# Performance work log

Hardware: AMD Instinct MI355X
Metric: run time of the kernel (lower is better)

## Reference

```python
import jax, jax.numpy as jnp
import numpy as np

B, T = 256, 1024
IN_DIM, OUT_DIM = 32, 32
STATE_DIM, DIM_NL = 128, 128
EPS = 1e-3            # pos_def_tol
ALPHA = 1.0           # contraction_rate_lb
STD = 0.5             # initialization_std


def setup_inputs() -> dict:
    key = jax.random.key(0)
    ks = jax.random.split(key, 9)
    f = lambda k, sh: jax.random.normal(k, sh, dtype=jnp.float32)
    n, q = STATE_DIM, DIM_NL
    return {
        "x0_sys": f(ks[0], (B, 1, OUT_DIM)),
        "u_in": f(ks[1], (B, T, IN_DIM)),
        "X": f(ks[2], (2 * n + q, 2 * n + q)) * STD,
        "Y": f(ks[3], (n, n)) * STD,
        "B2": f(ks[4], (n, IN_DIM)) * STD,
        "C2": f(ks[5], (OUT_DIM, n)) * STD,
        "D21": f(ks[6], (OUT_DIM, q)) * STD,
        "D22": f(ks[7], (OUT_DIM, IN_DIM)) * STD,
        "D12": f(ks[8], (q, IN_DIM)) * STD,
    }


def _derived(X, Y):
    # Contraction-preserving reparametrization ("_update_model_param").
    n, q = STATE_DIM, DIM_NL
    H = X.T @ X + EPS * jnp.eye(2 * n + q, dtype=X.dtype)
    H11 = H[:n, :n]
    H21 = H[n:n + q, :n]
    H22 = H[n:n + q, n:n + q]
    H31 = H[n + q:, :n]
    H32 = H[n + q:, n:n + q]
    H33 = H[n + q:, n + q:]          # P
    F_ = H31
    B1 = H32
    E = 0.5 * (H11 + ALPHA * H33 + Y - Y.T)
    E_inv = jnp.linalg.inv(E)
    Lam = 0.5 * jnp.diag(H22)
    D11 = -jnp.tril(H22, -1)          # strictly lower triangular
    C1 = -H21
    return F_, B1, E_inv, Lam, D11, C1


def reference(x0_sys, u_in, X, Y, B2, C2, D21, D22, D12):
    F_, B1, E_inv, Lam, D11, C1 = _derived(X, Y)
    q = DIM_NL

    # reset(): x0 = min-norm lstsq solution of C2 x0 = y0_sys  (lstsq == pinv here)
    y0_sys = x0_sys[:, 0, :]                       # (B, out)
    x0 = (jnp.linalg.pinv(C2) @ y0_sys.T).T        # (B, n)
    y0 = x0 @ C2.T                                 # (B, out)

    idx = jnp.arange(q)

    def step(x, u):
        # one REN forward step; x:(B,n), u:(B,in)
        a = x @ C1.T + u @ D12.T                   # (B, q), i-independent part of v

        def inner(w, inp):
            i, d_row, lam, a_i = inp               # a_i:(B,)
            v = a_i + w @ d_row                    # strictly-lower-tri recurrence on w
            return w.at[:, i].set(jnp.tanh(v / lam)), None

        w0 = jnp.zeros((x.shape[0], q), x.dtype)
        w, _ = jax.lax.scan(inner, w0, (idx, D11, Lam, a.T))
        x_new = (x @ F_.T + w @ B1.T + u @ B2.T) @ E_inv.T
        y = x_new @ C2.T + w @ D21.T + u @ D22.T
        return x_new, y

    _, ys = jax.lax.scan(step, x0, jnp.swapaxes(u_in, 0, 1))   # (T, B, out)
    # run() emits y0 then outputs after u[0..T-2] (last step's y is dropped)
    y_traj = jnp.concatenate([y0[None], ys[:-1]], axis=0)      # (T, B, out)
    return jnp.swapaxes(y_traj, 0, 1)                          # (B, T, out)
```

## Files before the change

### kernel.cpp

```cpp
#include <hip/hip_runtime.h>
#include <hip/hip_bf16.h>

#define DEV static __device__ __forceinline__

constexpr int Tn = 1024;
constexpr float LOG2E = 1.4426950408889634f;

constexpr int OFF_H     = 0;
constexpr int OFF_E     = 147456;
constexpr int OFF_EINV  = 163840;
constexpr int OFF_M     = 180224;
constexpr int OFF_MINV  = 181248;
constexpr int OFF_GL2   = 182272;
constexpr int OFF_FH    = 182400;
constexpr int OFF_B1H   = 198784;
constexpr int OFF_B2H   = 215168;
constexpr int OFF_W0    = 219264;
constexpr int OFF_WC    = 223360;
constexpr int OFF_CF    = 227456;
constexpr int OFF_CB    = 243840;
constexpr int OFF_CB2   = 260224;
constexpr int OFF_PF    = 264320;
constexpr int OFF_PB    = 280704;
constexpr int OFF_PCF   = 297088;
constexpr int OFF_PCB   = 313472;
constexpr int OFF_SAB   = 329856;
constexpr int OFF_SB2   = 338048;
constexpr int OFF_BUQ   = 342144;
constexpr int OFF_D12Q  = 346240;
constexpr int OFF_SCB2  = 350336;
constexpr int OFF_WCS   = 354432;
constexpr int OFF_C2Y   = 358528;
constexpr int OFF_D21Y  = 362624;
constexpr int OFF_D22Y  = 366720;
constexpr int OFF_AUG   = 367744;
constexpr int OFF_AUG2  = 400512;
constexpr int OFF_X0    = 402560;
constexpr int OFF_A0    = 435328;
constexpr int WS_FLOATS = 468096;

__device__ __align__(16) float g_ws[WS_FLOATS];
__device__ int g_isf32;

DEV float ld(const void* p, size_t i, int f) {
  return f ? ((const float*)p)[i]
           : __bfloat162float(((const __hip_bfloat16*)p)[i]);
}
DEV float rdlane(float v, int l) {
  return __int_as_float(__builtin_amdgcn_readlane(__float_as_int(v), l));
}

__global__ void k_detect(const void* __restrict__ X) {
  if (threadIdx.x == 0) {
    const __hip_bfloat16* p = (const __hip_bfloat16*)X;
    int bad = 0;
    for (int i = 0; i < 512; ++i) {
      float v = __bfloat162float(p[i]);
      if (!(v > -1e6f && v < 1e6f)) bad++;
    }
    g_isf32 = (bad > 0) ? 1 : 0;
  }
}

__global__ void k_H(const void* __restrict__ X) {
  const int f = g_isf32;
  float* ws = g_ws;
  int id = blockIdx.x * 256 + threadIdx.x;
  int r = id / 384, c = id % 384;
  float acc = 0.f;
  for (int k = 0; k < 384; ++k)
    acc = fmaf(ld(X, k * 384 + r, f), ld(X, k * 384 + c, f), acc);
  if (r == c) acc += 0.001f;
  ws[OFF_H + id] = acc;
}

__global__ void k_derived(const void* __restrict__ Y, const void* __restrict__ C2) {
  const int f = g_isf32;
  float* ws = g_ws;
  const float* H = ws + OFF_H;
  int id = blockIdx.x * 256 + threadIdx.x;
  if (id < 16384) {
    int i = id >> 7, j = id & 127;
    ws[OFF_E + id] = 0.5f * (H[i * 384 + j] + H[(256 + i) * 384 + 256 + j]
                             + ld(Y, i * 128 + j, f) - ld(Y, j * 128 + i, f));
  } else if (id < 16512) {
    int i = id - 16384;
    ws[OFF_GL2 + i] = LOG2E * 4.f / H[(128 + i) * 384 + 128 + i];
  } else if (id < 17536) {
    int t = id - 16512; int a = t >> 5, b = t & 31;
    float acc = 0.f;
    for (int j = 0; j < 128; ++j)
      acc = fmaf(ld(C2, a * 128 + j, f), ld(C2, b * 128 + j, f), acc);
    ws[OFF_M + t] = acc;
  }
}

__global__ void k_inv_lds() {
  extern __shared__ float smv[];
  float* aug  = smv;
  float* aug2 = smv + 32768;
  __shared__ float col[128];
  float* ws = g_ws;
  const float* E = ws + OFF_E;
  int tid = threadIdx.x;
  for (int idx = tid; idx < 32768; idx += 1024) {
    int i = idx >> 8, j = idx & 255;
    aug[idx] = (j < 128) ? E[i * 128 + j] : ((j - 128) == i ? 1.f : 0.f);
  }
  __syncthreads();
  for (int k = 0; k < 128; ++k) {
    if (tid < 128) col[tid] = aug[tid * 256 + k];
    __syncthreads();
    float d = 1.f / col[k];
    if (tid < 256) aug[k * 256 + tid] *= d;
    __syncthreads();
    int j = tid & 255, iseg = tid >> 8;
    float rkj = aug[k * 256 + j];
    for (int i = iseg * 32; i < iseg * 32 + 32; ++i) {
      if (i == k) continue;
      aug[i * 256 + j] -= col[i] * rkj;
    }
    __syncthreads();
  }
  for (int idx = tid; idx < 16384; idx += 1024) {
    int i = idx >> 7, j = idx & 127;
    ws[OFF_EINV + idx] = aug[i * 256 + 128 + j];
  }
  const float* M = ws + OFF_M;
  for (int idx = tid; idx < 2048; idx += 1024) {
    int i = idx >> 6, j = idx & 63;
    aug2[idx] = (j < 32) ? M[i * 32 + j] : ((j - 32) == i ? 1.f : 0.f);
  }
  __syncthreads();
  for (int k = 0; k < 32; ++k) {
    if (tid < 32) col[tid] = aug2[tid * 64 + k];
    __syncthreads();
    float d = 1.f / col[k];
    if (tid < 64) aug2[k * 64 + tid] *= d;
    __syncthreads();
    if (tid < 64) {
      float rkj = aug2[k * 64 + tid];
      for (int i = 0; i < 32; ++i) if (i != k) aug2[i * 64 + tid] -= col[i] * rkj;
    }
    __syncthreads();
  }
  for (int idx = tid; idx < 1024; idx += 1024) {
    int i = idx >> 5, j = idx & 31;
    ws[OFF_MINV + idx] = aug2[i * 64 + 32 + j];
  }
}

__global__ void k_inv() {
  float* ws = g_ws;
  __shared__ float col[128];
  float* aug = ws + OFF_AUG;
  const float* E = ws + OFF_E;
  int tid = threadIdx.x;
  for (int idx = tid; idx < 32768; idx += 1024) {
    int i = idx >> 8, j = idx & 255;
    aug[idx] = (j < 128) ? E[i * 128 + j] : ((j - 128) == i ? 1.f : 0.f);
  }
  __syncthreads();
  for (int k = 0; k < 128; ++k) {
    if (tid < 128) col[tid] = aug[tid * 256 + k];
    __syncthreads();
    float d = 1.f / col[k];
    if (tid < 256) aug[k * 256 + tid] *= d;
    __syncthreads();
    int j = tid & 255, iseg = tid >> 8;
    float rkj = aug[k * 256 + j];
    for (int i = iseg * 32; i < iseg * 32 + 32; ++i) {
      if (i == k) continue;
      aug[i * 256 + j] -= col[i] * rkj;
    }
    __syncthreads();
  }
  for (int idx = tid; idx < 16384; idx += 1024) {
    int i = idx >> 7, j = idx & 127;
    ws[OFF_EINV + idx] = aug[i * 256 + 128 + j];
  }
  __syncthreads();
  float* aug2 = ws + OFF_AUG2;
  const float* M = ws + OFF_M;
  for (int idx = tid; idx < 2048; idx += 1024) {
    int i = idx >> 6, j = idx & 63;
    aug2[idx] = (j < 32) ? M[i * 32 + j] : ((j - 32) == i ? 1.f : 0.f);
  }
  __syncthreads();
  for (int k = 0; k < 32; ++k) {
    if (tid < 32) col[tid] = aug2[tid * 64 + k];
    __syncthreads();
    float d = 1.f / col[k];
    if (tid < 64) aug2[k * 64 + tid] *= d;
    __syncthreads();
    if (tid < 64) {
      float rkj = aug2[k * 64 + tid];
      for (int i = 0; i < 32; ++i) if (i != k) aug2[i * 64 + tid] -= col[i] * rkj;
    }
    __syncthreads();
  }
  for (int idx = tid; idx < 1024; idx += 1024) {
    int i = idx >> 5, j = idx & 31;
    ws[OFF_MINV + idx] = aug2[i * 64 + 32 + j];
  }
}

__global__ void k_fuse(const void* __restrict__ B2, const void* __restrict__ C2) {
  const int f = g_isf32;
  float* ws = g_ws;
  const float* einv = ws + OFF_EINV;
  const float* H = ws + OFF_H;
  const float* minv = ws + OFF_MINV;
  int id = blockIdx.x * 256 + threadIdx.x;
  if (id < 16384) {
    int l = id >> 7, j = id & 127;
    float a = 0.f;
    for (int m = 0; m < 128; ++m) a = fmaf(einv[l * 128 + m], H[(256 + m) * 384 + j], a);
    ws[OFF_FH + id] = a;
  } else if (id < 32768) {
    int t = id - 16384; int l = t >> 7, j = t & 127;
    float a = 0.f;
    for (int m = 0; m < 128; ++m) a = fmaf(einv[l * 128 + m], H[(256 + m) * 384 + 128 + j], a);
    ws[OFF_B1H + t] = a;
  } else if (id < 36864) {
    int t = id - 32768; int l = t >> 5, k = t & 31;
    float a = 0.f;
    for (int m = 0; m < 128; ++m) a = fmaf(einv[l * 128 + m], ld(B2, m * 32 + k, f), a);
    ws[OFF_B2H + t] = a;
  } else if (id < 40960) {
    int t = id - 36864; int k = t >> 7, l = t & 127;
    float a = 0.f;
    for (int m = 0; m < 32; ++m) a = fmaf(minv[k * 32 + m], ld(C2, m * 128 + l, f), a);
    ws[OFF_W0 + t] = a;
  }
}

__global__ void k_w2() {
  float* ws = g_ws;
  const float* H = ws + OFF_H;
  const float* w0 = ws + OFF_W0;
  int id = blockIdx.x * 256 + threadIdx.x;
  int k = id >> 7, l = id & 127;
  float a = 0.f;
  for (int m = 0; m < 128; ++m) a = fmaf(w0[k * 128 + m], -H[(128 + l) * 384 + m], a);
  ws[OFF_WC + id] = a;
}

__global__ void k_cf() {
  float* ws = g_ws;
  const float* H = ws + OFF_H;
  int id = blockIdx.x * 256 + threadIdx.x;
  if (id < 16384) {
    int l = id >> 7, j = id & 127;
    float a = 0.f;
    for (int m = 0; m < 128; ++m) a = fmaf(-H[(128 + l) * 384 + m], ws[OFF_FH + m * 128 + j], a);
    ws[OFF_CF + id] = a;
  } else if (id < 32768) {
    int t = id - 16384; int l = t >> 7, j = t & 127;
    float a = 0.f;
    for (int m = 0; m < 128; ++m) a = fmaf(-H[(128 + l) * 384 + m], ws[OFF_B1H + m * 128 + j], a);
    ws[OFF_CB + t] = a;
  } else {
    int t = id - 32768; int l = t >> 5, k = t & 31;
    float a = 0.f;
    for (int m = 0; m < 128; ++m) a = fmaf(-H[(128 + l) * 384 + m], ws[OFF_B2H + m * 32 + k], a);
    ws[OFF_CB2 + t] = a;
  }
}

__global__ void k_pk(const void* __restrict__ D12, const void* __restrict__ C2,
                     const void* __restrict__ D21, const void* __restrict__ D22) {
  const int f = g_isf32;
  float* ws = g_ws;
  const float* H = ws + OFF_H;
  const float* g = ws + OFF_GL2;
  int id = blockIdx.x * 256 + threadIdx.x;
  if (id < 8192) {
    int j = id >> 6, l = id & 63;
    ((float2*)(ws + OFF_PF))[id] =
        make_float2(ws[OFF_FH + l * 128 + j], ws[OFF_FH + (l + 64) * 128 + j]);
  } else if (id < 16384) {
    int t = id - 8192; int j = t >> 6, l = t & 63;
    ((float2*)(ws + OFF_PB))[t] =
        make_float2(ws[OFF_B1H + l * 128 + j], ws[OFF_B1H + (l + 64) * 128 + j]);
  } else if (id < 24576) {
    int t = id - 16384; int j = t >> 6, l = t & 63;
    ((float2*)(ws + OFF_PCF))[t] =
        make_float2(g[l] * ws[OFF_CF + l * 128 + j], g[l + 64] * ws[OFF_CF + (l + 64) * 128 + j]);
  } else if (id < 32768) {
    int t = id - 24576; int j = t >> 6, l = t & 63;
    ((float2*)(ws + OFF_PCB))[t] =
        make_float2(g[l] * ws[OFF_CB + l * 128 + j], g[l + 64] * ws[OFF_CB + (l + 64) * 128 + j]);
  } else if (id < 36864) {
    int t = id - 32768; int i = t >> 6, l = t & 63;
    float sx = (i < l) ? -g[l] * H[(128 + l) * 384 + 128 + i] : 0.f;
    float sy = -g[l + 64] * H[(192 + l) * 384 + 128 + i];
    ((float2*)(ws + OFF_SAB))[t] = make_float2(sx, sy);
  } else if (id < 40960) {
    int t = id - 36864; int ii = t >> 6, l = t & 63;
    ws[OFF_SB2 + t] = (ii < l) ? -g[l + 64] * H[(192 + l) * 384 + 192 + ii] : 0.f;
  } else if (id < 43008) {
    int t = id - 40960; int k = t >> 6, l = t & 63;
    ((float2*)(ws + OFF_BUQ))[t] =
        make_float2(ws[OFF_B2H + l * 32 + k], ws[OFF_B2H + (l + 64) * 32 + k]);
  } else if (id < 45056) {
    int t = id - 43008; int k = t >> 6, l = t & 63;
    ((float2*)(ws + OFF_D12Q))[t] =
        make_float2(g[l] * ld(D12, l * 32 + k, f), g[l + 64] * ld(D12, (l + 64) * 32 + k, f));
  } else if (id < 47104) {
    int t = id - 45056; int k = t >> 6, l = t & 63;
    ((float2*)(ws + OFF_SCB2))[t] =
        make_float2(g[l] * ws[OFF_CB2 + l * 32 + k], g[l + 64] * ws[OFF_CB2 + (l + 64) * 32 + k]);
  } else if (id < 49152) {
    int t = id - 47104; int k = t >> 6, l = t & 63;
    ((float2*)(ws + OFF_WCS))[t] =
        make_float2(g[l] * ws[OFF_WC + k * 128 + l], g[l + 64] * ws[OFF_WC + k * 128 + l + 64]);
  } else if (id < 53248) {
    int t = id - 49152; int m = t >> 5, o = t & 31;
    ws[OFF_C2Y + t] = ld(C2, o * 128 + m, f);
  } else if (id < 57344) {
    int t = id - 53248; int m = t >> 5, o = t & 31;
    ws[OFF_D21Y + t] = ld(D21, o * 128 + m, f);
  } else if (id < 58368) {
    int t = id - 57344; int k = t >> 5, o = t & 31;
    ws[OFF_D22Y + t] = ld(D22, o * 32 + k, f);
  }
}

__global__ void k_x0a0(const void* __restrict__ x0s, const void* __restrict__ u_in) {
  const int f = g_isf32;
  float* ws = g_ws;
  int id = blockIdx.x * 256 + threadIdx.x;
  if (id < 32768) {
    int b = id >> 7, l = id & 127;
    float a = 0.f;
    for (int k = 0; k < 32; ++k)
      a = fmaf(ld(x0s, b * 32 + k, f), ws[OFF_W0 + k * 128 + l], a);
    ws[OFF_X0 + id] = a;
  } else {
    int t = id - 32768; int b = t >> 6, lane = t & 63;
    const float2* WCs = (const float2*)(ws + OFF_WCS);
    const float2* D12Q = (const float2*)(ws + OFF_D12Q);
    float ax = 0.f, ay = 0.f;
    for (int k = 0; k < 32; ++k) {
      float yk = ld(x0s, b * 32 + k, f);
      float2 wc = WCs[k * 64 + lane];
      ax = fmaf(wc.x, yk, ax); ay = fmaf(wc.y, yk, ay);
      float u0 = ld(u_in, b * Tn * 32 + k, f);
      float2 dq = D12Q[k * 64 + lane];
      ax = fmaf(dq.x, u0, ax); ay = fmaf(dq.y, u0, ay);
    }
    ((float2*)(ws + OFF_A0))[b * 64 + lane] = make_float2(ax, ay);
  }
}

DEV void y_emit(const float* ws, float xlv, float xhv, float2 wv, float uyv,
                int b, int t, int lane, int f, void* out) {
  int o = lane & 31, h = lane >> 5;
  const float* C2Y = ws + OFF_C2Y;
  const float* D21Y = ws + OFF_D21Y;
  const float* D22Y = ws + OFF_D22Y;
  float acc = 0.f;
#pragma unroll 8
  for (int l = 0; l < 64; ++l) {
    float xle = rdlane(xlv, l), xhe = rdlane(xhv, l);
    float xv = h ? xhe : xle;
    acc = fmaf(xv, C2Y[(l + 64 * h) * 32 + o], acc);
  }
#pragma unroll 8
  for (int l = 0; l < 64; ++l) {
    float wxe = rdlane(wv.x, l), wye = rdlane(wv.y, l);
    float wvv = h ? wye : wxe;
    acc = fmaf(wvv, D21Y[(l + 64 * h) * 32 + o], acc);
  }
  if (h == 0) {
#pragma unroll 8
    for (int k = 0; k < 32; ++k)
      acc = fmaf(rdlane(uyv, k), D22Y[k * 32 + o], acc);
  }
  acc += __shfl_down(acc, 32);
  if (lane < 32) {
    size_t oi = ((size_t)b * Tn + t) * 32 + o;
    if (f) ((float*)out)[oi] = acc;
    else   ((__hip_bfloat16*)out)[oi] = __float2bfloat16(acc);
  }
}

__global__ __launch_bounds__(512) void k_scan8(const void* __restrict__ u_in,
                                               const void* __restrict__ x0s,
                                               void* __restrict__ out) {
  __shared__ float2 sSAB[64 * 64];
  __shared__ float  sSB2[64 * 64];
  __shared__ float2 xbuf[2][8][64];
  __shared__ float2 abuf[2][8][64];
  const float* ws = g_ws;
  const int f = g_isf32;
  const int tid = threadIdx.x, lane = tid & 63, w = tid >> 6;
  for (int i = tid; i < 4096; i += 512) sSAB[i] = ((const float2*)(ws + OFF_SAB))[i];
  for (int i = tid; i < 4096; i += 512) sSB2[i] = ws[OFF_SB2 + i];

  const int b = blockIdx.x;
  const bool isScan = (w < 4);

  float2 vA[32], vB[32];
  if (isScan) {
    const float2* P1 = (const float2*)(ws + OFF_PB);
    const float2* P2 = (const float2*)(ws + OFF_PCB);
    const int jcol = (w & 3) * 32;
#pragma unroll
    for (int c = 0; c < 32; ++c) {
      vA[c] = P1[(jcol + c) * 64 + lane];
      vB[c] = P2[(jcol + c) * 64 + lane];
    }
  }
  float xl = ws[OFF_X0 + b * 128 + lane];
  float xh = ws[OFF_X0 + b * 128 + 64 + lane];
  float2 a2 = ((const float2*)(ws + OFF_A0))[b * 64 + lane];
  float accx = a2.x, accy = a2.y;

  float ucur = 0.f;
  float u0v = 0.f, u1v = 0.f;
  float uyc = 0.f;
  if (w == 4 && lane < 32) ucur = ld(u_in, (size_t)b * Tn * 32 + lane, f);
  if (w == 6 && lane < 32) {
    u0v = ld(u_in, (size_t)b * Tn * 32 + lane, f);
    u1v = ld(u_in, ((size_t)b * Tn + 1) * 32 + lane, f);
  }
  if (w == 6) { xbuf[0][6][lane] = make_float2(0.f, 0.f); xbuf[1][6][lane] = make_float2(0.f, 0.f); }
  if (w == 7 && lane < 32) {
    size_t oi = (size_t)b * Tn * 32 + lane;
    float v = ld(x0s, b * 32 + lane, f);
    if (f) ((float*)out)[oi] = v;
    else   ((__hip_bfloat16*)out)[oi] = __float2bfloat16(v);
  }
  const int jb = __builtin_amdgcn_readfirstlane((w & 1) * 32);
  __syncthreads();

#pragma unroll 1
  for (int t = 0; t < Tn - 1; ++t) {
    const int p = t & 1;
    if (isScan) {
      __builtin_amdgcn_s_setprio(1);
#pragma unroll
      for (int i = 0; i < 64; ++i) {
        float s = rdlane(accx, i);
        float e2 = __builtin_amdgcn_exp2f(s);
        float wi = fmaf(-2.f, __builtin_amdgcn_rcpf(1.f + e2), 1.f);
        float2 sp = sSAB[i * 64 + lane];
        accx = fmaf(sp.x, wi, accx);
        accy = fmaf(sp.y, wi, accy);
      }
      float ex = __builtin_amdgcn_exp2f(accx);
      float wx = fmaf(-2.f, __builtin_amdgcn_rcpf(1.f + ex), 1.f);
#pragma unroll
      for (int i = 0; i < 64; ++i) {
        float s = rdlane(accy, i);
        float e2 = __builtin_amdgcn_exp2f(s);
        float wi = fmaf(-2.f, __builtin_amdgcn_rcpf(1.f + e2), 1.f);
        accy = fmaf(sSB2[i * 64 + lane], wi, accy);
      }
      float ey = __builtin_amdgcn_exp2f(accy);
      float wy = fmaf(-2.f, __builtin_amdgcn_rcpf(1.f + ey), 1.f);
      if (w == 0) xbuf[p][7][lane] = make_float2(wx, wy);

      float px = 0.f, py = 0.f, pax = 0.f, pay = 0.f;
      float wsrc = (w < 2) ? wx : wy;
#pragma unroll
      for (int c = 0; c < 32; ++c) {
        float wj = rdlane(wsrc, jb + c);
        px  = fmaf(vA[c].x, wj, px);
        py  = fmaf(vA[c].y, wj, py);
        pax = fmaf(vB[c].x, wj, pax);
        pay = fmaf(vB[c].y, wj, pay);
      }
      __builtin_amdgcn_s_setprio(0);
      if (w != 0) xbuf[p][w][lane] = make_float2(px, py);
      else        xbuf[p][0][lane] = make_float2(px, py);
      abuf[p][w][lane] = make_float2(pax, pay);
      __syncthreads();
      float sax = 0.f, say = 0.f;
#pragma unroll
      for (int w2 = 0; w2 < 7; ++w2) {
        float2 av = abuf[p][w2][lane];
        sax += av.x; say += av.y;
      }
      accx = sax; accy = say;
    } else if (w == 4) {
      float un = ucur;
      if (lane < 32) un = ld(u_in, ((size_t)b * Tn + t + 1) * 32 + lane, f);
      float px = 0.f, py = 0.f, pax = 0.f, pay = 0.f;
      const float2* BUq = (const float2*)(ws + OFF_BUQ);
#pragma unroll 8
      for (int k = 0; k < 32; ++k) {
        float uk = rdlane(ucur, k);
        float2 bu = BUq[k * 64 + lane];
        px = fmaf(bu.x, uk, px); py = fmaf(bu.y, uk, py);
      }
      const float2* PF = (const float2*)(ws + OFF_PF);
      const float2* PCF = (const float2*)(ws + OFF_PCF);
#pragma unroll 8
      for (int c = 0; c < 64; ++c) {
        float xj = rdlane(xl, c);
        float2 fv = PF[c * 64 + lane];
        float2 cv = PCF[c * 64 + lane];
        px  = fmaf(fv.x, xj, px);  py  = fmaf(fv.y, xj, py);
        pax = fmaf(cv.x, xj, pax); pay = fmaf(cv.y, xj, pay);
      }
      ucur = un;
      xbuf[p][4][lane] = make_float2(px, py);
      abuf[p][4][lane] = make_float2(pax, pay);
      __syncthreads();
      float sxl = 0.f, sxh = 0.f;
#pragma unroll
      for (int w2 = 0; w2 < 7; ++w2) {
        float2 xv = xbuf[p][w2][lane];
        sxl += xv.x; sxh += xv.y;
      }
      xl = sxl; xh = sxh;
    } else if (w == 5) {
      float px = 0.f, py = 0.f, pax = 0.f, pay = 0.f;
      const float2* PF = (const float2*)(ws + OFF_PF);
      const float2* PCF = (const float2*)(ws + OFF_PCF);
#pragma unroll 8
      for (int c = 0; c < 64; ++c) {
        float xj = rdlane(xh, c);
        float2 fv = PF[(64 + c) * 64 + lane];
        float2 cv = PCF[(64 + c) * 64 + lane];
        px  = fmaf(fv.x, xj, px);  py  = fmaf(fv.y, xj, py);
        pax = fmaf(cv.x, xj, pax); pay = fmaf(cv.y, xj, pay);
      }
      xbuf[p][5][lane] = make_float2(px, py);
      abuf[p][5][lane] = make_float2(pax, pay);
      __syncthreads();
      float sxl = 0.f, sxh = 0.f;
#pragma unroll
      for (int w2 = 0; w2 < 7; ++w2) {
        float2 xv = xbuf[p][w2][lane];
        sxl += xv.x; sxh += xv.y;
      }
      xl = sxl; xh = sxh;
    } else if (w == 6) {
      float u2v = u1v;
      if (lane < 32 && t + 2 < Tn) u2v = ld(u_in, ((size_t)b * Tn + t + 2) * 32 + lane, f);
      float pax = 0.f, pay = 0.f;
      const float2* SC = (const float2*)(ws + OFF_SCB2);
      const float2* DQ = (const float2*)(ws + OFF_D12Q);
#pragma unroll 8
      for (int k = 0; k < 32; ++k) {
        float u0k = rdlane(u0v, k);
        float2 sc = SC[k * 64 + lane];
        pax = fmaf(sc.x, u0k, pax); pay = fmaf(sc.y, u0k, pay);
        float u1k = rdlane(u1v, k);
        float2 dq = DQ[k * 64 + lane];
        pax = fmaf(dq.x, u1k, pax); pay = fmaf(dq.y, u1k, pay);
      }
      u0v = u1v; u1v = u2v;
      abuf[p][6][lane] = make_float2(pax, pay);
      __syncthreads();
      float sxl = 0.f, sxh = 0.f;
#pragma unroll
      for (int w2 = 0; w2 < 7; ++w2) {
        float2 xv = xbuf[p][w2][lane];
        sxl += xv.x; sxh += xv.y;
      }
      xl = sxl; xh = sxh;
    } else {
      float uyn = uyc;
      if (lane < 32) uyn = ld(u_in, ((size_t)b * Tn + t) * 32 + lane, f);
      if (t >= 1) {
        float2 wv = xbuf[(t - 1) & 1][7][lane];
        y_emit(ws, xl, xh, wv, uyc, b, t, lane, f, out);
      }
      uyc = uyn;
      __syncthreads();
      float sxl = 0.f, sxh = 0.f;
#pragma unroll
      for (int w2 = 0; w2 < 7; ++w2) {
        float2 xv = xbuf[p][w2][lane];
        sxl += xv.x; sxh += xv.y;
      }
      xl = sxl; xh = sxh;
    }
  }
  if (w == 7) {
    float2 wv = xbuf[(Tn - 2) & 1][7][lane];
    y_emit(ws, xl, xh, wv, uyc, b, Tn - 1, lane, f, out);
  }
}

extern "C" void kernel_launch(void* const* d_in, const int* in_sizes, int n_in,
                              void* d_out, int out_size, void* d_ws, size_t ws_size,
                              hipStream_t stream) {
  const void* x0s = d_in[0];
  const void* u   = d_in[1];
  const void* X   = d_in[2];
  const void* Y   = d_in[3];
  const void* B2  = d_in[4];
  const void* C2  = d_in[5];
  const void* D21 = d_in[6];
  const void* D22 = d_in[7];
  const void* D12 = d_in[8];
  (void)d_ws; (void)ws_size; (void)in_sizes; (void)n_in; (void)out_size;

  hipLaunchKernelGGL(k_detect,  dim3(1),     dim3(64),   0, stream, X);
  hipLaunchKernelGGL(k_H,       dim3(576),   dim3(256),  0, stream, X);
  hipLaunchKernelGGL(k_derived, dim3(69),    dim3(256),  0, stream, Y, C2);

  hipError_t e = hipFuncSetAttribute((const void*)k_inv_lds,
                                     hipFuncAttributeMaxDynamicSharedMemorySize,
                                     139264);
  if (e == hipSuccess) {
    hipLaunchKernelGGL(k_inv_lds, dim3(1), dim3(1024), 139264, stream);
  } else {
    (void)hipGetLastError();
    hipLaunchKernelGGL(k_inv,     dim3(1), dim3(1024), 0, stream);
  }

  hipLaunchKernelGGL(k_fuse,    dim3(160),   dim3(256),  0, stream, B2, C2);
  hipLaunchKernelGGL(k_w2,      dim3(16),    dim3(256),  0, stream);
  hipLaunchKernelGGL(k_cf,      dim3(144),   dim3(256),  0, stream);
  hipLaunchKernelGGL(k_pk,      dim3(228),   dim3(256),  0, stream, D12, C2, D21, D22);
  hipLaunchKernelGGL(k_x0a0,    dim3(192),   dim3(256),  0, stream, x0s, u);
  hipLaunchKernelGGL(k_scan8,   dim3(256),   dim3(512),  0, stream, u, x0s, d_out);
}
```

Before: 6.603 ms.

## Restructure scan kernel: single wave runs nonlinear recurrence, others split projections

Only wave 0 now runs the sequential tanh recurrence; before, four waves each computed it redundantly. The next pre-activation is computed speculatively from the rank-1 update so the exp/rcp chain no longer waits on a full accumulator readlane each iteration. The B1/CB projection work is spread over waves 1-7 after a barrier, and the state projection moves to waves 1-4. This adds a second barrier per step and serializes the w-projection behind the recurrence instead of overlapping it. It also drops the double-buffered x/a buffers and the preloaded register weights.

```diff
diff --git a/kernel.cpp b/kernel.cpp
--- a/kernel.cpp
+++ b/kernel.cpp
@@ -391,8 +391,9 @@
                                                void* __restrict__ out) {
   __shared__ float2 sSAB[64 * 64];
   __shared__ float  sSB2[64 * 64];
-  __shared__ float2 xbuf[2][8][64];
-  __shared__ float2 abuf[2][8][64];
+  __shared__ float2 xbuf[8][64];
+  __shared__ float2 abuf[8][64];
+  __shared__ float2 wbuf[2][64];
   const float* ws = g_ws;
   const int f = g_isf32;
   const int tid = threadIdx.x, lane = tid & 63, w = tid >> 6;
@@ -400,95 +401,94 @@
   for (int i = tid; i < 4096; i += 512) sSB2[i] = ws[OFF_SB2 + i];
 
   const int b = blockIdx.x;
-  const bool isScan = (w < 4);
-
-  float2 vA[32], vB[32];
-  if (isScan) {
-    const float2* P1 = (const float2*)(ws + OFF_PB);
-    const float2* P2 = (const float2*)(ws + OFF_PCB);
-    const int jcol = (w & 3) * 32;
-#pragma unroll
-    for (int c = 0; c < 32; ++c) {
-      vA[c] = P1[(jcol + c) * 64 + lane];
-      vB[c] = P2[(jcol + c) * 64 + lane];
-    }
-  }
   float xl = ws[OFF_X0 + b * 128 + lane];
   float xh = ws[OFF_X0 + b * 128 + 64 + lane];
-  float2 a2 = ((const float2*)(ws + OFF_A0))[b * 64 + lane];
-  float accx = a2.x, accy = a2.y;
-
+  float accx = 0.f, accy = 0.f;
+  if (w == 0) {
+    float2 a2 = ((const float2*)(ws + OFF_A0))[b * 64 + lane];
+    accx = a2.x; accy = a2.y;
+    __builtin_amdgcn_s_setprio(1);
+  }
   float ucur = 0.f;
   float u0v = 0.f, u1v = 0.f;
   float uyc = 0.f;
-  if (w == 4 && lane < 32) ucur = ld(u_in, (size_t)b * Tn * 32 + lane, f);
+  if (w == 5 && lane < 32) ucur = ld(u_in, (size_t)b * Tn * 32 + lane, f);
   if (w == 6 && lane < 32) {
     u0v = ld(u_in, (size_t)b * Tn * 32 + lane, f);
     u1v = ld(u_in, ((size_t)b * Tn + 1) * 32 + lane, f);
   }
-  if (w == 6) { xbuf[0][6][lane] = make_float2(0.f, 0.f); xbuf[1][6][lane] = make_float2(0.f, 0.f); }
   if (w == 7 && lane < 32) {
     size_t oi = (size_t)b * Tn * 32 + lane;
     float v = ld(x0s, b * 32 + lane, f);
     if (f) ((float*)out)[oi] = v;
     else   ((__hip_bfloat16*)out)[oi] = __float2bfloat16(v);
   }
-  const int jb = __builtin_amdgcn_readfirstlane((w & 1) * 32);
+  int jst_, cnt_;
+  if (w <= 4)       { jst_ = (w - 1) * 16; cnt_ = 16; }
+  else if (w == 5)  { jst_ = 64;  cnt_ = 24; }
+  else if (w == 6)  { jst_ = 88;  cnt_ = 24; }
+  else              { jst_ = 112; cnt_ = 16; }
+  const int jst = __builtin_amdgcn_readfirstlane(jst_);
+  const int cnt = __builtin_amdgcn_readfirstlane(cnt_);
+  const int lb2 = __builtin_amdgcn_readfirstlane((w <= 4) ? jst_ : jst_ - 64);
   __syncthreads();
 
 #pragma unroll 1
   for (int t = 0; t < Tn - 1; ++t) {
     const int p = t & 1;
-    if (isScan) {
-      __builtin_amdgcn_s_setprio(1);
+    float px = 0.f, py = 0.f, pax = 0.f, pay = 0.f;
+    if (w == 0) {
+      float s = rdlane(accx, 0);
 #pragma unroll
       for (int i = 0; i < 64; ++i) {
-        float s = rdlane(accx, i);
         float e2 = __builtin_amdgcn_exp2f(s);
-        float wi = fmaf(-2.f, __builtin_amdgcn_rcpf(1.f + e2), 1.f);
+        float r  = __builtin_amdgcn_rcpf(1.f + e2);
+        float wi = fmaf(-2.f, r, 1.f);
         float2 sp = sSAB[i * 64 + lane];
+        if (i < 63) {
+          float spn  = rdlane(sp.x, i + 1);
+          float sold = rdlane(accx, i + 1);
+          s = fmaf(spn, wi, sold);
+        }
         accx = fmaf(sp.x, wi, accx);
         accy = fmaf(sp.y, wi, accy);
       }
       float ex = __builtin_amdgcn_exp2f(accx);
-      float wx = fmaf(-2.f, __builtin_amdgcn_rcpf(1.f + ex), 1.f);
+      float wxv = fmaf(-2.f, __builtin_amdgcn_rcpf(1.f + ex), 1.f);
+      float s2 = rdlane(accy, 0);
 #pragma unroll
       for (int i = 0; i < 64; ++i) {
-        float s = rdlane(accy, i);
-        float e2 = __builtin_amdgcn_exp2f(s);
-        float wi = fmaf(-2.f, __builtin_amdgcn_rcpf(1.f + e2), 1.f);
-        accy = fmaf(sSB2[i * 64 + lane], wi, accy);
+        float e2 = __builtin_amdgcn_exp2f(s2);
+        float r  = __builtin_amdgcn_rcpf(1.f + e2);
+        float wi = fmaf(-2.f, r, 1.f);
+        float sb = sSB2[i * 64 + lane];
+        if (i < 63) {
+          float spn  = rdlane(sb, i + 1);
+          float sold = rdlane(accy, i + 1);
+          s2 = fmaf(spn, wi, sold);
+        }
+        accy = fmaf(sb, wi, accy);
       }
       float ey = __builtin_amdgcn_exp2f(accy);
-      float wy = fmaf(-2.f, __builtin_amdgcn_rcpf(1.f + ey), 1.f);
-      if (w == 0) xbuf[p][7][lane] = make_float2(wx, wy);
-
-      float px = 0.f, py = 0.f, pax = 0.f, pay = 0.f;
-      float wsrc = (w < 2) ? wx : wy;
-#pragma unroll
+      float wyv = fmaf(-2.f, __builtin_amdgcn_rcpf(1.f + ey), 1.f);
+      wbuf[p][lane] = make_float2(wxv, wyv);
+    } else if (w <= 4) {
+      const float2* PF  = (const float2*)(ws + OFF_PF);
+      const float2* PCF = (const float2*)(ws + OFF_PCF);
+      float xsrc = (w <= 2) ? xl : xh;
+      const int jcb = (w - 1) * 32;
+      const int lb1 = __builtin_amdgcn_readfirstlane(((w - 1) & 1) * 32);
+#pragma unroll 8
       for (int c = 0; c < 32; ++c) {
-        float wj = rdlane(wsrc, jb + c);
-        px  = fmaf(vA[c].x, wj, px);
-        py  = fmaf(vA[c].y, wj, py);
-        pax = fmaf(vB[c].x, wj, pax);
-        pay = fmaf(vB[c].y, wj, pay);
-      }
-      __builtin_amdgcn_s_setprio(0);
-      if (w != 0) xbuf[p][w][lane] = make_float2(px, py);
-      else        xbuf[p][0][lane] = make_float2(px, py);
-      abuf[p][w][lane] = make_float2(pax, pay);
-      __syncthreads();
-      float sax = 0.f, say = 0.f;
-#pragma unroll
-      for (int w2 = 0; w2 < 7; ++w2) {
-        float2 av = abuf[p][w2][lane];
-        sax += av.x; say += av.y;
-      }
-      accx = sax; accy = say;
-    } else if (w == 4) {
+        float xj = rdlane(xsrc, lb1 + c);
+        float2 fv = PF[(jcb + c) * 64 + lane];
+        float2 cv = PCF[(jcb + c) * 64 + lane];
+        px  = fmaf(fv.x, xj, px);  py  = fmaf(fv.y, xj, py);
+        pax = fmaf(cv.x, xj, pax); pay = fmaf(cv.y, xj, pay);
+      }
+    } else if (w == 5) {
       float un = ucur;
       if (lane < 32) un = ld(u_in, ((size_t)b * Tn + t + 1) * 32 + lane, f);
-      float px = 0.f, py = 0.f, pax = 0.f, pay = 0.f;
       const float2* BUq = (const float2*)(ws + OFF_BUQ);
 #pragma unroll 8
       for (int k = 0; k < 32; ++k) {
@@ -496,53 +496,10 @@
         float2 bu = BUq[k * 64 + lane];
         px = fmaf(bu.x, uk, px); py = fmaf(bu.y, uk, py);
       }
-      const float2* PF = (const float2*)(ws + OFF_PF);
-      const float2* PCF = (const float2*)(ws + OFF_PCF);
-#pragma unroll 8
-      for (int c = 0; c < 64; ++c) {
-        float xj = rdlane(xl, c);
-        float2 fv = PF[c * 64 + lane];
-        float2 cv = PCF[c * 64 + lane];
-        px  = fmaf(fv.x, xj, px);  py  = fmaf(fv.y, xj, py);
-        pax = fmaf(cv.x, xj, pax); pay = fmaf(cv.y, xj, pay);
-      }
       ucur = un;
-      xbuf[p][4][lane] = make_float2(px, py);
-      abuf[p][4][lane] = make_float2(pax, pay);
-      __syncthreads();
-      float sxl = 0.f, sxh = 0.f;
-#pragma unroll
-      for (int w2 = 0; w2 < 7; ++w2) {
-        float2 xv = xbuf[p][w2][lane];
-        sxl += xv.x; sxh += xv.y;
-      }
-      xl = sxl; xh = sxh;
-    } else if (w == 5) {
-      float px = 0.f, py = 0.f, pax = 0.f, pay = 0.f;
-      const float2* PF = (const float2*)(ws + OFF_PF);
-      const float2* PCF = (const float2*)(ws + OFF_PCF);
-#pragma unroll 8
-      for (int c = 0; c < 64; ++c) {
-        float xj = rdlane(xh, c);
-        float2 fv = PF[(64 + c) * 64 + lane];
-        float2 cv = PCF[(64 + c) * 64 + lane];
-        px  = fmaf(fv.x, xj, px);  py  = fmaf(fv.y, xj, py);
-        pax = fmaf(cv.x, xj, pax); pay = fmaf(cv.y, xj, pay);
-      }
-      xbuf[p][5][lane] = make_float2(px, py);
-      abuf[p][5][lane] = make_float2(pax, pay);
-      __syncthreads();
-      float sxl = 0.f, sxh = 0.f;
-#pragma unroll
-      for (int w2 = 0; w2 < 7; ++w2) {
-        float2 xv = xbuf[p][w2][lane];
-        sxl += xv.x; sxh += xv.y;
-      }
-      xl = sxl; xh = sxh;
     } else if (w == 6) {
       float u2v = u1v;
       if (lane < 32 && t + 2 < Tn) u2v = ld(u_in, ((size_t)b * Tn + t + 2) * 32 + lane, f);
-      float pax = 0.f, pay = 0.f;
       const float2* SC = (const float2*)(ws + OFF_SCB2);
       const float2* DQ = (const float2*)(ws + OFF_D12Q);
 #pragma unroll 8
@@ -555,35 +512,54 @@
         pax = fmaf(dq.x, u1k, pax); pay = fmaf(dq.y, u1k, pay);
       }
       u0v = u1v; u1v = u2v;
-      abuf[p][6][lane] = make_float2(pax, pay);
-      __syncthreads();
-      float sxl = 0.f, sxh = 0.f;
-#pragma unroll
-      for (int w2 = 0; w2 < 7; ++w2) {
-        float2 xv = xbuf[p][w2][lane];
-        sxl += xv.x; sxh += xv.y;
-      }
-      xl = sxl; xh = sxh;
     } else {
       float uyn = uyc;
       if (lane < 32) uyn = ld(u_in, ((size_t)b * Tn + t) * 32 + lane, f);
       if (t >= 1) {
-        float2 wv = xbuf[(t - 1) & 1][7][lane];
+        float2 wv = wbuf[(t - 1) & 1][lane];
         y_emit(ws, xl, xh, wv, uyc, b, t, lane, f, out);
       }
       uyc = uyn;
-      __syncthreads();
+    }
+    __syncthreads();
+
+    if (w != 0) {
+      float2 wv2 = wbuf[p][lane];
+      float wsrc = (w <= 4) ? wv2.x : wv2.y;
+      const float2* PB  = (const float2*)(ws + OFF_PB);
+      const float2* PCB = (const float2*)(ws + OFF_PCB);
+      for (int c = 0; c < cnt; ++c) {
+        float wj = rdlane(wsrc, lb2 + c);
+        float2 bv = PB[(jst + c) * 64 + lane];
+        float2 cv = PCB[(jst + c) * 64 + lane];
+        px  = fmaf(bv.x, wj, px);  py  = fmaf(bv.y, wj, py);
+        pax = fmaf(cv.x, wj, pax); pay = fmaf(cv.y, wj, pay);
+      }
+      xbuf[w][lane] = make_float2(px, py);
+      abuf[w][lane] = make_float2(pax, pay);
+    }
+    __syncthreads();
+
+    if (w == 0) {
+      float sax = 0.f, say = 0.f;
+#pragma unroll
+      for (int w2 = 1; w2 < 8; ++w2) {
+        float2 av = abuf[w2][lane];
+        sax += av.x; say += av.y;
+      }
+      accx = sax; accy = say;
+    } else if (w <= 4 || w == 7) {
       float sxl = 0.f, sxh = 0.f;
 #pragma unroll
-      for (int w2 = 0; w2 < 7; ++w2) {
-        float2 xv = xbuf[p][w2][lane];
+      for (int w2 = 1; w2 < 8; ++w2) {
+        float2 xv = xbuf[w2][lane];
         sxl += xv.x; sxh += xv.y;
       }
       xl = sxl; xh = sxh;
     }
   }
   if (w == 7) {
-    float2 wv = xbuf[(Tn - 2) & 1][7][lane];
+    float2 wv = wbuf[(Tn - 2) & 1][lane];
     y_emit(ws, xl, xh, wv, uyc, b, Tn - 1, lane, f, out);
   }
 }
```

After: 10.11 ms. 53.2% more time.

## Rebalance scan kernel warps and stage all weight matrices in dynamic LDS

Applied to the files above, without the earlier changes.

Adds a new scan kernel that keeps all per-step weight matrices (BUQ, SCB2, D12Q, C2Y, D21Y, D22Y) in dynamic shared memory instead of reading them from global memory each step. It also reassigns the non-scan warps: warps 4-7 now each hold a slice of the F/CF projection in registers and split the x-side matvec. This frees warp 6 from its previous role and moves the output emission onto warp 7. All eight warps then contribute partial sums through shared buffers. The old kernel is kept as a fallback if the large dynamic LDS allocation is refused. The goals are less global-memory latency per step and more even warp load, at the cost of higher register use and more LDS traffic per step.

```diff
diff --git a/kernel.cpp b/kernel.cpp
--- a/kernel.cpp
+++ b/kernel.cpp
@@ -386,9 +386,226 @@
   }
 }
 
-__global__ __launch_bounds__(512) void k_scan8(const void* __restrict__ u_in,
-                                               const void* __restrict__ x0s,
-                                               void* __restrict__ out) {
+DEV void y_emit_l(const float* sC2Y, const float* sD21Y, const float* sD22Y,
+                  float xlv, float xhv, float2 wv, float uyv,
+                  int b, int t, int lane, int f, void* out) {
+  int o = lane & 31, h = lane >> 5;
+  float acc = 0.f;
+#pragma unroll 8
+  for (int l = 0; l < 64; ++l) {
+    float xle = rdlane(xlv, l), xhe = rdlane(xhv, l);
+    float xv = h ? xhe : xle;
+    acc = fmaf(xv, sC2Y[(l + 64 * h) * 32 + o], acc);
+  }
+#pragma unroll 8
+  for (int l = 0; l < 64; ++l) {
+    float wxe = rdlane(wv.x, l), wye = rdlane(wv.y, l);
+    float wvv = h ? wye : wxe;
+    acc = fmaf(wvv, sD21Y[(l + 64 * h) * 32 + o], acc);
+  }
+  if (h == 0) {
+#pragma unroll 8
+    for (int k = 0; k < 32; ++k)
+      acc = fmaf(rdlane(uyv, k), sD22Y[k * 32 + o], acc);
+  }
+  acc += __shfl_down(acc, 32);
+  if (lane < 32) {
+    size_t oi = ((size_t)b * Tn + t) * 32 + o;
+    if (f) ((float*)out)[oi] = acc;
+    else   ((__hip_bfloat16*)out)[oi] = __float2bfloat16(acc);
+  }
+}
+
+__global__ __launch_bounds__(512, 2) void k_scan8m(const void* __restrict__ u_in,
+                                                   const void* __restrict__ x0s,
+                                                   void* __restrict__ out) {
+  extern __shared__ float sm[];
+  float2* sSAB  = (float2*)sm;
+  float*  sSB2  = sm + 8192;
+  float2* xbuf  = (float2*)(sm + 12288);
+  float2* abuf  = (float2*)(sm + 14336);
+  float2* wbuf  = (float2*)(sm + 16384);
+  float2* sBUQ  = (float2*)(sm + 16640);
+  float2* sSCB2 = (float2*)(sm + 20736);
+  float2* sD12Q = (float2*)(sm + 24832);
+  float*  sC2Y  = sm + 28928;
+  float*  sD21Y = sm + 33024;
+  float*  sD22Y = sm + 37120;
+  const float* ws = g_ws;
+  const int f = g_isf32;
+  const int tid = threadIdx.x, lane = tid & 63, w = tid >> 6;
+  for (int i = tid; i < 4096; i += 512) sSAB[i] = ((const float2*)(ws + OFF_SAB))[i];
+  for (int i = tid; i < 4096; i += 512) sSB2[i] = ws[OFF_SB2 + i];
+  for (int i = tid; i < 2048; i += 512) sBUQ[i] = ((const float2*)(ws + OFF_BUQ))[i];
+  for (int i = tid; i < 2048; i += 512) sSCB2[i] = ((const float2*)(ws + OFF_SCB2))[i];
+  for (int i = tid; i < 2048; i += 512) sD12Q[i] = ((const float2*)(ws + OFF_D12Q))[i];
+  for (int i = tid; i < 4096; i += 512) sC2Y[i] = ws[OFF_C2Y + i];
+  for (int i = tid; i < 4096; i += 512) sD21Y[i] = ws[OFF_D21Y + i];
+  for (int i = tid; i < 1024; i += 512) sD22Y[i] = ws[OFF_D22Y + i];
+
+  const int b = blockIdx.x;
+  const bool isScan = (w < 4);
+
+  float2 vA[32], vB[32];
+  {
+    const float2* P1 = (const float2*)(ws + (isScan ? OFF_PB : OFF_PF));
+    const float2* P2 = (const float2*)(ws + (isScan ? OFF_PCB : OFF_PCF));
+    const int jcol = (w & 3) * 32;
+#pragma unroll
+    for (int c = 0; c < 32; ++c) {
+      vA[c] = P1[(jcol + c) * 64 + lane];
+      vB[c] = P2[(jcol + c) * 64 + lane];
+    }
+  }
+  float xl = ws[OFF_X0 + b * 128 + lane];
+  float xh = ws[OFF_X0 + b * 128 + 64 + lane];
+  float accx = 0.f, accy = 0.f;
+  if (isScan) {
+    float2 a2 = ((const float2*)(ws + OFF_A0))[b * 64 + lane];
+    accx = a2.x; accy = a2.y;
+  }
+  float ucur = 0.f;
+  float u0v = 0.f, u1v = 0.f;
+  float uyc = 0.f;
+  if (w == 4 && lane < 32) ucur = ld(u_in, (size_t)b * Tn * 32 + lane, f);
+  if (w == 5 && lane < 32) {
+    u0v = ld(u_in, (size_t)b * Tn * 32 + lane, f);
+    u1v = ld(u_in, ((size_t)b * Tn + 1) * 32 + lane, f);
+  }
+  if (w == 7 && lane < 32) {
+    size_t oi = (size_t)b * Tn * 32 + lane;
+    float v = ld(x0s, b * 32 + lane, f);
+    if (f) ((float*)out)[oi] = v;
+    else   ((__hip_bfloat16*)out)[oi] = __float2bfloat16(v);
+  }
+  const int jb = __builtin_amdgcn_readfirstlane((w & 1) * 32);
+  __syncthreads();
+
+#pragma unroll 1
+  for (int t = 0; t < Tn - 1; ++t) {
+    const int p = t & 1;
+    if (isScan) {
+      __builtin_amdgcn_s_setprio(1);
+      float s = rdlane(accx, 0);
+#pragma unroll
+      for (int i = 0; i < 64; ++i) {
+        float e2 = __builtin_amdgcn_exp2f(s);
+        float r  = __builtin_amdgcn_rcpf(1.f + e2);
+        float wi = fmaf(-2.f, r, 1.f);
+        float2 sp = sSAB[i * 64 + lane];
+        if (i < 63) {
+          float spn  = rdlane(sp.x, i + 1);
+          float sold = rdlane(accx, i + 1);
+          s = fmaf(spn, wi, sold);
+        }
+        accx = fmaf(sp.x, wi, accx);
+        accy = fmaf(sp.y, wi, accy);
+      }
+      float ex = __builtin_amdgcn_exp2f(accx);
+      float wxv = fmaf(-2.f, __builtin_amdgcn_rcpf(1.f + ex), 1.f);
+      float s2 = rdlane(accy, 0);
+#pragma unroll
+      for (int i = 0; i < 64; ++i) {
+        float e2 = __builtin_amdgcn_exp2f(s2);
+        float r  = __builtin_amdgcn_rcpf(1.f + e2);
+        float wi = fmaf(-2.f, r, 1.f);
+        float sb = sSB2[i * 64 + lane];
+        if (i < 63) {
+          float spn  = rdlane(sb, i + 1);
+          float sold = rdlane(accy, i + 1);
+          s2 = fmaf(spn, wi, sold);
+        }
+        accy = fmaf(sb, wi, accy);
+      }
+      float ey = __builtin_amdgcn_exp2f(accy);
+      float wyv = fmaf(-2.f, __builtin_amdgcn_rcpf(1.f + ey), 1.f);
+      if (w == 0) wbuf[p * 64 + lane] = make_float2(wxv, wyv);
+
+      float px = 0.f, py = 0.f, pax = 0.f, pay = 0.f;
+      float wsrc = (w < 2) ? wxv : wyv;
+#pragma unroll
+      for (int c = 0; c < 32; ++c) {
+        float wj = rdlane(wsrc, jb + c);
+        px  = fmaf(vA[c].x, wj, px);
+        py  = fmaf(vA[c].y, wj, py);
+        pax = fmaf(vB[c].x, wj, pax);
+        pay = fmaf(vB[c].y, wj, pay);
+      }
+      __builtin_amdgcn_s_setprio(0);
+      xbuf[(p * 8 + w) * 64 + lane] = make_float2(px, py);
+      abuf[(p * 8 + w) * 64 + lane] = make_float2(pax, pay);
+      __syncthreads();
+      float sax = 0.f, say = 0.f;
+#pragma unroll
+      for (int w2 = 0; w2 < 8; ++w2) {
+        float2 av = abuf[(p * 8 + w2) * 64 + lane];
+        sax += av.x; say += av.y;
+      }
+      accx = sax; accy = say;
+    } else {
+      float px = 0.f, py = 0.f, pax = 0.f, pay = 0.f;
+      if (w == 4) {
+        float un = ucur;
+        if (lane < 32) un = ld(u_in, ((size_t)b * Tn + t + 1) * 32 + lane, f);
+#pragma unroll 8
+        for (int k = 0; k < 32; ++k) {
+          float uk = rdlane(ucur, k);
+          float2 bu = sBUQ[k * 64 + lane];
+          px = fmaf(bu.x, uk, px); py = fmaf(bu.y, uk, py);
+        }
+        ucur = un;
+      } else if (w == 5) {
+        float u2v = u1v;
+        if (lane < 32 && t + 2 < Tn) u2v = ld(u_in, ((size_t)b * Tn + t + 2) * 32 + lane, f);
+#pragma unroll 8
+        for (int k = 0; k < 32; ++k) {
+          float u0k = rdlane(u0v, k);
+          float2 sc = sSCB2[k * 64 + lane];
+          pax = fmaf(sc.x, u0k, pax); pay = fmaf(sc.y, u0k, pay);
+          float u1k = rdlane(u1v, k);
+          float2 dq = sD12Q[k * 64 + lane];
+          pax = fmaf(dq.x, u1k, pax); pay = fmaf(dq.y, u1k, pay);
+        }
+        u0v = u1v; u1v = u2v;
+      } else if (w == 7) {
+        float uyn = uyc;
+        if (lane < 32) uyn = ld(u_in, ((size_t)b * Tn + t) * 32 + lane, f);
+        if (t >= 1) {
+          float2 wv = wbuf[((t - 1) & 1) * 64 + lane];
+          y_emit_l(sC2Y, sD21Y, sD22Y, xl, xh, wv, uyc, b, t, lane, f, out);
+        }
+        uyc = uyn;
+      }
+      float xsrc = (w < 6) ? xl : xh;
+#pragma unroll
+      for (int c = 0; c < 32; ++c) {
+        float xj = rdlane(xsrc, jb + c);
+        px  = fmaf(vA[c].x, xj, px);
+        py  = fmaf(vA[c].y, xj, py);
+        pax = fmaf(vB[c].x, xj, pax);
+        pay = fmaf(vB[c].y, xj, pay);
+      }
+      xbuf[(p * 8 + w) * 64 + lane] = make_float2(px, py);
+      abuf[(p * 8 + w) * 64 + lane] = make_float2(pax, pay);
+      __syncthreads();
+      float sxl = 0.f, sxh = 0.f;
+#pragma unroll
+      for (int w2 = 0; w2 < 8; ++w2) {
+        float2 xv = xbuf[(p * 8 + w2) * 64 + lane];
+        sxl += xv.x; sxh += xv.y;
+      }
+      xl = sxl; xh = sxh;
+    }
+  }
+  if (w == 7) {
+    float2 wv = wbuf[((Tn - 2) & 1) * 64 + lane];
+    y_emit_l(sC2Y, sD21Y, sD22Y, xl, xh, wv, uyc, b, Tn - 1, lane, f, out);
+  }
+}
+
+__global__ __launch_bounds__(512) void k_scan8_fb(const void* __restrict__ u_in,
+                                                  const void* __restrict__ x0s,
+                                                  void* __restrict__ out) {
   __shared__ float2 sSAB[64 * 64];
   __shared__ float  sSB2[64 * 64];
   __shared__ float2 xbuf[2][8][64];
@@ -401,7 +618,6 @@
 
   const int b = blockIdx.x;
   const bool isScan = (w < 4);
-
   float2 vA[32], vB[32];
   if (isScan) {
     const float2* P1 = (const float2*)(ws + OFF_PB);
@@ -417,7 +633,6 @@
   float xh = ws[OFF_X0 + b * 128 + 64 + lane];
   float2 a2 = ((const float2*)(ws + OFF_A0))[b * 64 + lane];
   float accx = a2.x, accy = a2.y;
-
   float ucur = 0.f;
   float u0v = 0.f, u1v = 0.f;
   float uyc = 0.f;
@@ -474,8 +689,7 @@
         pay = fmaf(vB[c].y, wj, pay);
       }
       __builtin_amdgcn_s_setprio(0);
-      if (w != 0) xbuf[p][w][lane] = make_float2(px, py);
-      else        xbuf[p][0][lane] = make_float2(px, py);
+      xbuf[p][w][lane] = make_float2(px, py);
       abuf[p][w][lane] = make_float2(pax, pay);
       __syncthreads();
       float sax = 0.f, say = 0.f;
@@ -621,5 +835,14 @@
   hipLaunchKernelGGL(k_cf,      dim3(144),   dim3(256),  0, stream);
   hipLaunchKernelGGL(k_pk,      dim3(228),   dim3(256),  0, stream, D12, C2, D21, D22);
   hipLaunchKernelGGL(k_x0a0,    dim3(192),   dim3(256),  0, stream, x0s, u);
-  hipLaunchKernelGGL(k_scan8,   dim3(256),   dim3(512),  0, stream, u, x0s, d_out);
-}
+
+  hipError_t e2 = hipFuncSetAttribute((const void*)k_scan8m,
+                                      hipFuncAttributeMaxDynamicSharedMemorySize,
+                                      152576);
+  if (e2 == hipSuccess) {
+    hipLaunchKernelGGL(k_scan8m, dim3(256), dim3(512), 152576, stream, u, x0s, d_out);
+  } else {
+    (void)hipGetLastError();
+    hipLaunchKernelGGL(k_scan8_fb, dim3(256), dim3(512), 0, stream, u, x0s, d_out);
+  }
+}
```

Measured after the change: 6.940 ms. +5.1%, slower.
